# Optimization experiments

Hardware: AMD Instinct MI355X
Metric: run time of the kernel (lower is better)

Reference implementation:

```python
import jax, jax.numpy as jnp
import numpy as np

N_DOWN, N_ABOVE, D_IN, D_OUT, FAN_IN = 50000, 100000, 256, 256, 5


def setup_inputs() -> dict:
    key = jax.random.key(0)
    ks = jax.random.split(key, 8)
    h = jax.random.normal(ks[0], (N_DOWN, D_IN), dtype=jnp.float32)
    h_above = jax.random.normal(ks[1], (N_ABOVE, D_IN), dtype=jnp.float32)  # only shape[0] used
    # idx: unique positions of the down nodes within the up-node index space
    idx = jax.random.permutation(ks[2], N_ABOVE)[:N_DOWN]
    # fixed fan-in 5: destination ids i are each node repeated 5 times (DGL bucketing order)
    i = jnp.repeat(jnp.arange(N_ABOVE), FAN_IN)
    j = jax.random.randint(ks[3], (N_ABOVE * FAN_IN,), 0, N_ABOVE)
    s1 = 1.0 / np.sqrt(D_IN * FAN_IN)
    s2 = 1.0 / np.sqrt(D_OUT)
    W1 = jax.random.uniform(ks[4], (D_IN * FAN_IN, D_OUT), jnp.float32, -s1, s1)
    b1 = jax.random.uniform(ks[5], (D_OUT,), jnp.float32, -s1, s1)
    W2 = jax.random.uniform(ks[6], (D_OUT, D_OUT), jnp.float32, -s2, s2)
    b2 = jax.random.uniform(ks[7], (D_OUT,), jnp.float32, -s2, s2)
    return {"h": h, "h_above": h_above, "idx": idx, "i": i, "j": j,
            "W1": W1, "b1": b1, "W2": W2, "b2": b2}


def reference(h, h_above, idx, i, j, W1, b1, W2, b2):
    n_above = h_above.shape[0]
    d = h.shape[1]
    # scatter down-node features into the up-node index space (new_h[idx] = h)
    new_h = jnp.zeros((n_above, d), dtype=h.dtype).at[idx].set(h)
    # gather the 5 source-node messages per destination; i = repeat(arange, 5),
    # so j grouped in blocks of 5 corresponds to each destination's mailbox.
    gathered = new_h[j].reshape(n_above, 5 * d)  # [n_above, 5*d]
    hid = jax.nn.relu(gathered @ W1 + b1)
    return hid @ W2 + b2
```

## Files before the change

kernel.cpp:

```cpp
#include <hip/hip_runtime.h>

#define N_DOWN  50000
#define N_ABOVE 100000
#define DIM     256
#define FAN     5
#define K1      1280
#define MPAD    100096

typedef __bf16 bf16x8 __attribute__((ext_vector_type(8)));
typedef float  f32x4  __attribute__((ext_vector_type(4)));

__device__ __forceinline__ unsigned short f2bf(float f) {
  unsigned u = __builtin_bit_cast(unsigned, f);
  u += 0x7FFFu + ((u >> 16) & 1u);
  return (unsigned short)(u >> 16);
}

__device__ __forceinline__ void gload16(const unsigned short* g, unsigned short* l) {
  __builtin_amdgcn_global_load_lds(
      (const __attribute__((address_space(1))) void*)g,
      (__attribute__((address_space(3))) void*)l, 16, 0, 0);
}

__global__ void k_prep_inv(int* __restrict__ inv, unsigned short* __restrict__ hbf) {
  int t = blockIdx.x * 256 + threadIdx.x;
  if (t < N_ABOVE) inv[t] = N_DOWN;
  if (t < DIM)     hbf[(size_t)N_DOWN * DIM + t] = 0;
}

__global__ void k_scatter(const int* __restrict__ idx, int* __restrict__ inv) {
  int t = blockIdx.x * 256 + threadIdx.x;
  if (t < N_DOWN) inv[idx[t]] = t;
}

__global__ void k_h2bf(const float* __restrict__ h, unsigned short* __restrict__ hbf) {
  int t = blockIdx.x * 256 + threadIdx.x;
  float4 v = ((const float4*)h)[t];
  ushort4 o;
  o.x = f2bf(v.x); o.y = f2bf(v.y); o.z = f2bf(v.z); o.w = f2bf(v.w);
  ((ushort4*)hbf)[t] = o;
}

__global__ void k_transpose_bf(const float* __restrict__ in, unsigned short* __restrict__ out,
                               int K, int N) {
  __shared__ float tile[64][65];
  int k0 = blockIdx.x * 64, n0 = blockIdx.y * 64;
  int c = threadIdx.x & 63, rb = threadIdx.x >> 6;
#pragma unroll
  for (int rr = 0; rr < 16; ++rr) {
    int row = rb + rr * 4;
    tile[row][c] = in[(size_t)(k0 + row) * N + n0 + c];
  }
  __syncthreads();
#pragma unroll
  for (int rr = 0; rr < 16; ++rr) {
    int nr = rb + rr * 4;
    out[(size_t)(n0 + nr) * K + k0 + c] = f2bf(tile[c][nr]);
  }
}

__global__ __launch_bounds__(256, 2) void k_gemm1(
    const unsigned short* __restrict__ hbf,
    const unsigned short* __restrict__ w1t,
    const float* __restrict__ b1,
    const int* __restrict__ inv,
    const int* __restrict__ jarr,
    unsigned short* __restrict__ hid)
{
  __shared__ __align__(16) unsigned short Alds[128 * 64];
  __shared__ __align__(16) unsigned short Blds[128 * 64];
  __shared__ int srcrow[128 * FAN];

  const int tid = threadIdx.x;
  const int w = tid >> 6, l = tid & 63;
  const int m0 = blockIdx.x * 128, n0 = blockIdx.y * 128;
  const int wm = w >> 1, wn = w & 1;
  const int srow = l >> 3, slot = l & 7;

  for (int e = tid; e < 128 * FAN; e += 256) {
    int row = e / FAN, rr = e - row * FAN;
    int gm = m0 + row;
    int s = N_DOWN;
    if (gm < N_ABOVE) s = inv[jarr[(size_t)gm * FAN + rr]];
    srcrow[e] = s;
  }

  f32x4 acc[4][4] = {};

  for (int t = 0; t < 20; ++t) {
    const int r = t >> 2;
    __syncthreads();
#pragma unroll
    for (int i = 0; i < 4; ++i) {
      int row = w * 32 + i * 8 + srow;
      int src = srcrow[row * FAN + r];
      int c = slot ^ (row & 7);
      gload16(hbf + ((size_t)src << 8) + ((t & 3) << 6) + (c << 3),
              Alds + (w * 32 + i * 8) * 64);
    }
#pragma unroll
    for (int i = 0; i < 4; ++i) {
      int row = w * 32 + i * 8 + srow;
      int c = slot ^ (row & 7);
      gload16(w1t + (size_t)(n0 + row) * K1 + (t << 6) + (c << 3),
              Blds + (w * 32 + i * 8) * 64);
    }
    __syncthreads();

#pragma unroll
    for (int kk = 0; kk < 2; ++kk) {
      bf16x8 af[4], bfr[4];
#pragma unroll
      for (int m = 0; m < 4; ++m) {
        int row = wm * 64 + m * 16 + (l & 15);
        int c = (kk * 4 + (l >> 4)) ^ (row & 7);
        af[m] = *(const bf16x8*)(Alds + row * 64 + c * 8);
      }
#pragma unroll
      for (int n = 0; n < 4; ++n) {
        int row = wn * 64 + n * 16 + (l & 15);
        int c = (kk * 4 + (l >> 4)) ^ (row & 7);
        bfr[n] = *(const bf16x8*)(Blds + row * 64 + c * 8);
      }
#pragma unroll
      for (int m = 0; m < 4; ++m)
#pragma unroll
        for (int n = 0; n < 4; ++n)
          acc[m][n] = __builtin_amdgcn_mfma_f32_16x16x32_bf16(af[m], bfr[n], acc[m][n], 0, 0, 0);
    }
  }

#pragma unroll
  for (int n = 0; n < 4; ++n) {
    int gn = n0 + wn * 64 + n * 16 + (l & 15);
    float bias = b1[gn];
#pragma unroll
    for (int m = 0; m < 4; ++m) {
      int gm0 = m0 + wm * 64 + m * 16 + (l >> 4) * 4;
#pragma unroll
      for (int q = 0; q < 4; ++q) {
        float v = acc[m][n][q] + bias;
        v = v > 0.f ? v : 0.f;
        hid[(size_t)(gm0 + q) * DIM + gn] = f2bf(v);
      }
    }
  }
}

__global__ __launch_bounds__(256, 2) void k_gemm2(
    const unsigned short* __restrict__ hid,
    const unsigned short* __restrict__ w2t,
    const float* __restrict__ b2,
    float* __restrict__ out)
{
  __shared__ __align__(16) unsigned short Alds[128 * 64];
  __shared__ __align__(16) unsigned short Blds[128 * 64];

  const int tid = threadIdx.x;
  const int w = tid >> 6, l = tid & 63;
  const int m0 = blockIdx.x * 128, n0 = blockIdx.y * 128;
  const int wm = w >> 1, wn = w & 1;
  const int srow = l >> 3, slot = l & 7;

  f32x4 acc[4][4] = {};

  for (int t = 0; t < 4; ++t) {
    __syncthreads();
#pragma unroll
    for (int i = 0; i < 4; ++i) {
      int row = w * 32 + i * 8 + srow;
      int c = slot ^ (row & 7);
      gload16(hid + (size_t)(m0 + row) * DIM + (t << 6) + (c << 3),
              Alds + (w * 32 + i * 8) * 64);
      gload16(w2t + (size_t)(n0 + row) * DIM + (t << 6) + (c << 3),
              Blds + (w * 32 + i * 8) * 64);
    }
    __syncthreads();

#pragma unroll
    for (int kk = 0; kk < 2; ++kk) {
      bf16x8 af[4], bfr[4];
#pragma unroll
      for (int m = 0; m < 4; ++m) {
        int row = wm * 64 + m * 16 + (l & 15);
        int c = (kk * 4 + (l >> 4)) ^ (row & 7);
        af[m] = *(const bf16x8*)(Alds + row * 64 + c * 8);
      }
#pragma unroll
      for (int n = 0; n < 4; ++n) {
        int row = wn * 64 + n * 16 + (l & 15);
        int c = (kk * 4 + (l >> 4)) ^ (row & 7);
        bfr[n] = *(const bf16x8*)(Blds + row * 64 + c * 8);
      }
#pragma unroll
      for (int m = 0; m < 4; ++m)
#pragma unroll
        for (int n = 0; n < 4; ++n)
          acc[m][n] = __builtin_amdgcn_mfma_f32_16x16x32_bf16(af[m], bfr[n], acc[m][n], 0, 0, 0);
    }
  }

#pragma unroll
  for (int n = 0; n < 4; ++n) {
    int gn = n0 + wn * 64 + n * 16 + (l & 15);
    float bias = b2[gn];
#pragma unroll
    for (int m = 0; m < 4; ++m) {
      int gm0 = m0 + wm * 64 + m * 16 + (l >> 4) * 4;
#pragma unroll
      for (int q = 0; q < 4; ++q) {
        int gm = gm0 + q;
        if (gm < N_ABOVE) out[(size_t)gm * DIM + gn] = acc[m][n][q] + bias;
      }
    }
  }
}

extern "C" void kernel_launch(void* const* d_in, const int* in_sizes, int n_in,
                              void* d_out, int out_size, void* d_ws, size_t ws_size,
                              hipStream_t stream) {
  const float* h    = (const float*)d_in[0];
  const int*   idx  = (const int*)d_in[2];
  const int*   jarr = (const int*)d_in[4];
  const float* W1   = (const float*)d_in[5];
  const float* b1   = (const float*)d_in[6];
  const float* W2   = (const float*)d_in[7];
  const float* b2   = (const float*)d_in[8];
  float* out = (float*)d_out;

  char* ws = (char*)d_ws;
  size_t off = 0;
  auto alloc = [&](size_t bytes) -> void* {
    void* p = ws + off;
    off += bytes;
    off = (off + 511) & ~(size_t)511;
    return p;
  };
  int*            inv = (int*)alloc((size_t)N_ABOVE * 4);
  unsigned short* hbf = (unsigned short*)alloc((size_t)(N_DOWN + 1) * DIM * 2);
  unsigned short* w1t = (unsigned short*)alloc((size_t)DIM * K1 * 2);
  unsigned short* w2t = (unsigned short*)alloc((size_t)DIM * DIM * 2);
  unsigned short* hid = (unsigned short*)alloc((size_t)MPAD * DIM * 2);
  if (ws_size < off) return;

  k_prep_inv<<<dim3(391), dim3(256), 0, stream>>>(inv, hbf);
  k_scatter<<<dim3(196), dim3(256), 0, stream>>>(idx, inv);
  k_h2bf<<<dim3(12500), dim3(256), 0, stream>>>(h, hbf);
  k_transpose_bf<<<dim3(K1 / 64, DIM / 64), dim3(256), 0, stream>>>(W1, w1t, K1, DIM);
  k_transpose_bf<<<dim3(DIM / 64, DIM / 64), dim3(256), 0, stream>>>(W2, w2t, DIM, DIM);
  k_gemm1<<<dim3(MPAD / 128, 2), dim3(256), 0, stream>>>(hbf, w1t, b1, inv, jarr, hid);
  k_gemm2<<<dim3(MPAD / 128, 2), dim3(256), 0, stream>>>(hid, w2t, b2, out);
}
```

Baseline: 142.8 us.

## Merge prep kernels into one launch and widen gemm2 to full N per block

The scatter, h-to-bf16 conversion and both weight transposes now run as one kernel that picks its role from the block index, which removes three launches and the gaps between them. gemm2 now uses 512-thread blocks that cover all 256 output columns, so each block loads its hid tile once instead of twice. The epilogues of both GEMMs are reordered to hoist the bias loads and iterate n innermost. The price is a larger LDS footprint and more registers per gemm2 block, which may limit occupancy.

```diff
diff --git a/kernel.cpp b/kernel.cpp
--- a/kernel.cpp
+++ b/kernel.cpp
@@ -28,23 +28,10 @@
   if (t < DIM)     hbf[(size_t)N_DOWN * DIM + t] = 0;
 }
 
-__global__ void k_scatter(const int* __restrict__ idx, int* __restrict__ inv) {
-  int t = blockIdx.x * 256 + threadIdx.x;
-  if (t < N_DOWN) inv[idx[t]] = t;
-}
-
-__global__ void k_h2bf(const float* __restrict__ h, unsigned short* __restrict__ hbf) {
-  int t = blockIdx.x * 256 + threadIdx.x;
-  float4 v = ((const float4*)h)[t];
-  ushort4 o;
-  o.x = f2bf(v.x); o.y = f2bf(v.y); o.z = f2bf(v.z); o.w = f2bf(v.w);
-  ((ushort4*)hbf)[t] = o;
-}
-
-__global__ void k_transpose_bf(const float* __restrict__ in, unsigned short* __restrict__ out,
-                               int K, int N) {
-  __shared__ float tile[64][65];
-  int k0 = blockIdx.x * 64, n0 = blockIdx.y * 64;
+__device__ __forceinline__ void transpose_tile(const float* __restrict__ in,
+                                               unsigned short* __restrict__ out,
+                                               int K, int N, int k0, int n0,
+                                               float (*tile)[65]) {
   int c = threadIdx.x & 63, rb = threadIdx.x >> 6;
 #pragma unroll
   for (int rr = 0; rr < 16; ++rr) {
@@ -56,6 +43,30 @@
   for (int rr = 0; rr < 16; ++rr) {
     int nr = rb + rr * 4;
     out[(size_t)(n0 + nr) * K + k0 + c] = f2bf(tile[c][nr]);
+  }
+}
+
+__global__ void k_prep_all(const float* __restrict__ h, const int* __restrict__ idx,
+                           const float* __restrict__ W1, const float* __restrict__ W2,
+                           int* __restrict__ inv, unsigned short* __restrict__ hbf,
+                           unsigned short* __restrict__ w1t, unsigned short* __restrict__ w2t) {
+  __shared__ float tile[64][65];
+  const int b = blockIdx.x;
+  if (b < 12500) {
+    int t = b * 256 + threadIdx.x;
+    float4 v = ((const float4*)h)[t];
+    ushort4 o;
+    o.x = f2bf(v.x); o.y = f2bf(v.y); o.z = f2bf(v.z); o.w = f2bf(v.w);
+    ((ushort4*)hbf)[t] = o;
+  } else if (b < 12696) {
+    int t = (b - 12500) * 256 + threadIdx.x;
+    if (t < N_DOWN) inv[idx[t]] = t;
+  } else if (b < 12776) {
+    int bb = b - 12696;
+    transpose_tile(W1, w1t, K1, DIM, (bb % 20) * 64, (bb / 20) * 64, tile);
+  } else {
+    int bb = b - 12776;
+    transpose_tile(W2, w2t, DIM, DIM, (bb % 4) * 64, (bb / 4) * 64, tile);
   }
 }
 
@@ -130,49 +141,58 @@
     }
   }
 
-#pragma unroll
-  for (int n = 0; n < 4; ++n) {
-    int gn = n0 + wn * 64 + n * 16 + (l & 15);
-    float bias = b1[gn];
-#pragma unroll
-    for (int m = 0; m < 4; ++m) {
-      int gm0 = m0 + wm * 64 + m * 16 + (l >> 4) * 4;
-#pragma unroll
-      for (int q = 0; q < 4; ++q) {
+  float bias0 = b1[n0 + wn * 64 + 0 * 16 + (l & 15)];
+  float bias1 = b1[n0 + wn * 64 + 1 * 16 + (l & 15)];
+  float bias2 = b1[n0 + wn * 64 + 2 * 16 + (l & 15)];
+  float bias3 = b1[n0 + wn * 64 + 3 * 16 + (l & 15)];
+#pragma unroll
+  for (int m = 0; m < 4; ++m) {
+#pragma unroll
+    for (int q = 0; q < 4; ++q) {
+      int gm = m0 + wm * 64 + m * 16 + (l >> 4) * 4 + q;
+#pragma unroll
+      for (int n = 0; n < 4; ++n) {
+        float bias = n == 0 ? bias0 : n == 1 ? bias1 : n == 2 ? bias2 : bias3;
+        int gn = n0 + wn * 64 + n * 16 + (l & 15);
         float v = acc[m][n][q] + bias;
         v = v > 0.f ? v : 0.f;
-        hid[(size_t)(gm0 + q) * DIM + gn] = f2bf(v);
-      }
-    }
-  }
-}
-
-__global__ __launch_bounds__(256, 2) void k_gemm2(
+        hid[(size_t)gm * DIM + gn] = f2bf(v);
+      }
+    }
+  }
+}
+
+__global__ __launch_bounds__(512, 2) void k_gemm2(
     const unsigned short* __restrict__ hid,
     const unsigned short* __restrict__ w2t,
     const float* __restrict__ b2,
     float* __restrict__ out)
 {
   __shared__ __align__(16) unsigned short Alds[128 * 64];
-  __shared__ __align__(16) unsigned short Blds[128 * 64];
+  __shared__ __align__(16) unsigned short Blds[256 * 64];
 
   const int tid = threadIdx.x;
   const int w = tid >> 6, l = tid & 63;
-  const int m0 = blockIdx.x * 128, n0 = blockIdx.y * 128;
-  const int wm = w >> 1, wn = w & 1;
+  const int m0 = blockIdx.x * 128;
+  const int wm = w >> 2, wn = w & 3;
   const int srow = l >> 3, slot = l & 7;
 
   f32x4 acc[4][4] = {};
 
   for (int t = 0; t < 4; ++t) {
     __syncthreads();
+#pragma unroll
+    for (int i = 0; i < 2; ++i) {
+      int row = w * 16 + i * 8 + srow;
+      int c = slot ^ (row & 7);
+      gload16(hid + (size_t)(m0 + row) * DIM + (t << 6) + (c << 3),
+              Alds + (w * 16 + i * 8) * 64);
+    }
 #pragma unroll
     for (int i = 0; i < 4; ++i) {
       int row = w * 32 + i * 8 + srow;
       int c = slot ^ (row & 7);
-      gload16(hid + (size_t)(m0 + row) * DIM + (t << 6) + (c << 3),
-              Alds + (w * 32 + i * 8) * 64);
-      gload16(w2t + (size_t)(n0 + row) * DIM + (t << 6) + (c << 3),
+      gload16(w2t + (size_t)row * DIM + (t << 6) + (c << 3),
               Blds + (w * 32 + i * 8) * 64);
     }
     __syncthreads();
@@ -200,17 +220,22 @@
     }
   }
 
-#pragma unroll
-  for (int n = 0; n < 4; ++n) {
-    int gn = n0 + wn * 64 + n * 16 + (l & 15);
-    float bias = b2[gn];
-#pragma unroll
-    for (int m = 0; m < 4; ++m) {
-      int gm0 = m0 + wm * 64 + m * 16 + (l >> 4) * 4;
-#pragma unroll
-      for (int q = 0; q < 4; ++q) {
-        int gm = gm0 + q;
-        if (gm < N_ABOVE) out[(size_t)gm * DIM + gn] = acc[m][n][q] + bias;
+  float bias0 = b2[wn * 64 + 0 * 16 + (l & 15)];
+  float bias1 = b2[wn * 64 + 1 * 16 + (l & 15)];
+  float bias2 = b2[wn * 64 + 2 * 16 + (l & 15)];
+  float bias3 = b2[wn * 64 + 3 * 16 + (l & 15)];
+#pragma unroll
+  for (int m = 0; m < 4; ++m) {
+#pragma unroll
+    for (int q = 0; q < 4; ++q) {
+      int gm = m0 + wm * 64 + m * 16 + (l >> 4) * 4 + q;
+      if (gm < N_ABOVE) {
+#pragma unroll
+        for (int n = 0; n < 4; ++n) {
+          float bias = n == 0 ? bias0 : n == 1 ? bias1 : n == 2 ? bias2 : bias3;
+          int gn = wn * 64 + n * 16 + (l & 15);
+          out[(size_t)gm * DIM + gn] = acc[m][n][q] + bias;
+        }
       }
     }
   }
@@ -244,10 +269,7 @@
   if (ws_size < off) return;
 
   k_prep_inv<<<dim3(391), dim3(256), 0, stream>>>(inv, hbf);
-  k_scatter<<<dim3(196), dim3(256), 0, stream>>>(idx, inv);
-  k_h2bf<<<dim3(12500), dim3(256), 0, stream>>>(h, hbf);
-  k_transpose_bf<<<dim3(K1 / 64, DIM / 64), dim3(256), 0, stream>>>(W1, w1t, K1, DIM);
-  k_transpose_bf<<<dim3(DIM / 64, DIM / 64), dim3(256), 0, stream>>>(W2, w2t, DIM, DIM);
+  k_prep_all<<<dim3(12792), dim3(256), 0, stream>>>(h, idx, W1, W2, inv, hbf, w1t, w2t);
   k_gemm1<<<dim3(MPAD / 128, 2), dim3(256), 0, stream>>>(hbf, w1t, b1, inv, jarr, hid);
-  k_gemm2<<<dim3(MPAD / 128, 2), dim3(256), 0, stream>>>(hid, w2t, b2, out);
-}
+  k_gemm2<<<dim3(MPAD / 128), dim3(512), 0, stream>>>(hid, w2t, b2, out);
+}
```

Result: faster. 124.4 us, median of 2 (-12.8%).
